# Optimization experiments

Measured on AMD Instinct MI355X. Metric: run time of the kernel, lower is better.

The kernel has to match this reference:

```python
import jax, jax.numpy as jnp
import numpy as np

C_IN = 256
C_INT = C_IN // 2  # inter_channels


def _conv1x1(x, w, b):
    # x: [B, Cin, H, W], w: [Cout, Cin], b: [Cout]
    return jnp.einsum('bchw,oc->bohw', x, w) + b[None, :, None, None]


def setup_inputs() -> dict:
    key = jax.random.key(0)
    ks = jax.random.split(key, 9)
    B, H, W = 8, 64, 64
    s_in = 1.0 / np.sqrt(C_IN)
    s_int = 1.0 / np.sqrt(C_INT)
    return {
        'x': jax.random.normal(ks[0], (B, C_IN, H, W), dtype=jnp.float32),
        'g_w': jax.random.normal(ks[1], (C_INT, C_IN), dtype=jnp.float32) * s_in,
        'g_b': jax.random.normal(ks[2], (C_INT,), dtype=jnp.float32) * s_in,
        'theta_w': jax.random.normal(ks[3], (C_INT, C_IN), dtype=jnp.float32) * s_in,
        'theta_b': jax.random.normal(ks[4], (C_INT,), dtype=jnp.float32) * s_in,
        'phi_w': jax.random.normal(ks[5], (C_INT, C_IN), dtype=jnp.float32) * s_in,
        'phi_b': jax.random.normal(ks[6], (C_INT,), dtype=jnp.float32) * s_in,
        'W_w': jax.random.normal(ks[7], (C_IN, C_INT), dtype=jnp.float32) * s_int,
        'W_b': jax.random.normal(ks[8], (C_IN,), dtype=jnp.float32) * s_int,
    }


def reference(x, g_w, g_b, theta_w, theta_b, phi_w, phi_b, W_w, W_b):
    B, C, H, W = x.shape
    N = H * W
    g_x = _conv1x1(x, g_w, g_b).reshape(B, C_INT, N)        # [B, Ci, N]
    theta_x = _conv1x1(x, theta_w, theta_b).reshape(B, C_INT, N)
    phi_x = _conv1x1(x, phi_w, phi_b).reshape(B, C_INT, N)
    # f[b, i, j] = theta[:, i] . phi[:, j]  (no scaling, per original)
    f = jnp.einsum('bci,bcj->bij', theta_x, phi_x)          # [B, N, N]
    f_div_C = jax.nn.softmax(f, axis=-1)
    y = jnp.einsum('bij,bcj->bci', f_div_C, g_x)            # [B, Ci, N]
    y = y.reshape(B, C_INT, H, W)
    y = _conv1x1(y, W_w, W_b)                               # [B, C, H, W]
    return x + y
```

## Files before the change

kernel.cpp:

```cpp
#include <hip/hip_runtime.h>

typedef _Float16 f16;
typedef _Float16 f16x2 __attribute__((ext_vector_type(2)));
typedef _Float16 f16x4 __attribute__((ext_vector_type(4)));
typedef _Float16 f16x8 __attribute__((ext_vector_type(8)));
typedef float f32x4 __attribute__((ext_vector_type(4)));
typedef float f32x16 __attribute__((ext_vector_type(16)));

#define MFMA16(a, b, c) __builtin_amdgcn_mfma_f32_16x16x32_f16(a, b, c, 0, 0, 0)
#define MFMA32(a, b, c) __builtin_amdgcn_mfma_f32_32x32x16_f16(a, b, c, 0, 0, 0)

__device__ __forceinline__ int swzr(int row) { return ((row & 7) << 4) ^ ((row & 8) << 2); }

__global__ __launch_bounds__(256) void wcvt_k(
    const float* __restrict__ tw, const float* __restrict__ pw,
    const float* __restrict__ gw, const float* __restrict__ ww,
    f16* __restrict__ Wall, f16* __restrict__ Wepi) {
  int i = blockIdx.x * 256 + threadIdx.x;
  if (i < 384 * 256) {
    int c = i >> 8, cp = i & 255;
    float v = (c < 128) ? tw[c * 256 + cp]
            : (c < 256) ? pw[(c - 128) * 256 + cp]
                        : gw[(c - 256) * 256 + cp];
    Wall[i] = (f16)v;
  }
  int j = i - 384 * 256;
  if (j >= 0 && j < 256 * 128) Wepi[j] = (f16)ww[j];
}

__global__ __launch_bounds__(256) void xpose_k(const float* __restrict__ x,
                                               f16* __restrict__ xT) {
  __shared__ f16 t[64 * 65];
  int bx = blockIdx.x;
  int b = bx >> 8, rem = bx & 255;
  int c0 = (rem >> 6) * 64, n0 = (rem & 63) * 64;
  const float* xb = x + ((size_t)b * 256 + c0) * 4096 + n0;
#pragma unroll
  for (int rep = 0; rep < 16; ++rep) {
    int idx = rep * 256 + threadIdx.x;
    int i = idx >> 6, j = idx & 63;
    t[j * 65 + i] = (f16)xb[(size_t)i * 4096 + j];
  }
  __syncthreads();
  f16* o = xT + ((size_t)b * 4096 + n0) * 256 + c0;
#pragma unroll
  for (int rep = 0; rep < 16; ++rep) {
    int idx = rep * 256 + threadIdx.x;
    int j = idx >> 6, i = idx & 63;
    o[(size_t)j * 256 + i] = t[j * 65 + i];
  }
}

__global__ __launch_bounds__(256) void proj_k(
    const f16* __restrict__ xT, const f16* __restrict__ Wall,
    const float* __restrict__ tb, const float* __restrict__ pb,
    const float* __restrict__ gb, f16* __restrict__ Q, f16* __restrict__ K,
    f16* __restrict__ Vt) {
  __shared__ f16 vs[128 * 65];
  int b = blockIdx.x >> 6, nt = blockIdx.x & 63;
  int nbase = nt * 64;
  int w = threadIdx.x >> 6, lane = threadIdx.x & 63;
  int lr = lane & 15, lhi = lane >> 4;
  int nrow = nbase + w * 16 + lr;
  const f16x8* xr = (const f16x8*)(xT + ((size_t)b * 4096 + nrow) * 256);
  f16x8 a[8];
#pragma unroll
  for (int ks = 0; ks < 8; ++ks) a[ks] = xr[ks * 4 + lhi];
  f32x4 acc[24];
#pragma unroll
  for (int ct = 0; ct < 24; ++ct) {
    acc[ct] = {0.f, 0.f, 0.f, 0.f};
    const f16x8* wr = (const f16x8*)(Wall + (size_t)(ct * 16 + lr) * 256);
#pragma unroll
    for (int ks = 0; ks < 8; ++ks) acc[ct] = MFMA16(a[ks], wr[ks * 4 + lhi], acc[ct]);
  }
  int nloc = w * 16 + lhi * 4;
#pragma unroll
  for (int ct = 0; ct < 24; ++ct) {
    int c = ct * 16 + lr;
    float bias = (c < 128) ? tb[c] : (c < 256) ? pb[c - 128] : gb[c - 256];
#pragma unroll
    for (int r = 0; r < 4; ++r) {
      float v = acc[ct][r] + bias;
      int n = nbase + nloc + r;
      if (c < 128)
        Q[((size_t)b * 4096 + n) * 128 + c] = (f16)v;
      else if (c < 256)
        K[((size_t)b * 4096 + n) * 128 + (c - 128)] = (f16)v;
      else
        vs[(c - 256) * 65 + nloc + r] = (f16)v;
    }
  }
  __syncthreads();
  f16* vo = Vt + (size_t)b * 128 * 4096 + nbase;
  for (int rep = 0; rep < 32; ++rep) {
    int idx = rep * 256 + threadIdx.x;
    int c = idx >> 6, j = idx & 63;
    vo[(size_t)c * 4096 + j] = vs[c * 65 + j];
  }
}

__global__ __launch_bounds__(256, 2) void attn_k(const f16* __restrict__ Q,
                                                 const f16* __restrict__ K,
                                                 const f16* __restrict__ Vt,
                                                 f16* __restrict__ Yp,
                                                 float2* __restrict__ ml) {
  __shared__ f16 Ks[2][64 * 128];
  __shared__ f16 Vs[2][128 * 64];
  const float L = 1.44269504f;
  int swzid = ((blockIdx.x & 7) << 6) | ((int)blockIdx.x >> 3);
  int b = swzid >> 6, rem = swzid & 63;
  int qt = rem >> 1, half = rem & 1;
  int qbase = qt * 128;
  int kvbase = half * 2048;
  int tid = threadIdx.x;
  int w = tid >> 6, lane = tid & 63;
  int col = lane & 31, hi = lane >> 5;

  const f16* Qr = Q + ((size_t)b * 4096 + qbase + w * 32 + col) * 128;
  f16x8 bq[8];
#pragma unroll
  for (int ks = 0; ks < 8; ++ks) bq[ks] = *(const f16x8*)(Qr + ks * 16 + hi * 8);

  f32x16 yacc[4];
#pragma unroll
  for (int dt = 0; dt < 4; ++dt)
#pragma unroll
    for (int r = 0; r < 16; ++r) yacc[dt][r] = 0.f;
  float m = -1e30f, l = 0.f, nmL = 1e30f;

  const f16* Kbase = K + (size_t)b * 4096 * 128;
  const f16* Vbase = Vt + (size_t)b * 128 * 4096;

  int krow = tid >> 4, kcolb = (tid & 15) * 16;
  int vrow = tid >> 1, h2 = tid & 1;
  int sv = swzr(vrow);

  int vblo[4];
#pragma unroll
  for (int u = 0; u < 4; ++u) vblo[u] = h2 * 64 + (u & 2) * 16 + (u & 1) * 8;

  {
    const f16* Kt = Kbase + (size_t)kvbase * 128;
    f16x8 kr[4], vr[4];
#pragma unroll
    for (int r = 0; r < 4; ++r) kr[r] = *(const f16x8*)(Kt + (r * 256 + tid) * 8);
#pragma unroll
    for (int u = 0; u < 4; ++u)
      vr[u] = *(const f16x8*)(Vbase + (size_t)vrow * 4096 + kvbase + h2 * 32 + u * 8);
#pragma unroll
    for (int r = 0; r < 4; ++r) {
      int row = r * 16 + krow;
      *(f16x8*)((char*)Ks[0] + row * 256 + (kcolb ^ swzr(row))) = kr[r];
    }
#pragma unroll
    for (int u = 0; u < 4; ++u) {
      f16x4 lo = {vr[u][0], vr[u][1], vr[u][2], vr[u][3]};
      f16x4 hi4 = {vr[u][4], vr[u][5], vr[u][6], vr[u][7]};
      *(f16x4*)((char*)Vs[0] + vrow * 128 + (vblo[u] ^ sv)) = lo;
      *(f16x4*)((char*)Vs[0] + vrow * 128 + ((vblo[u] + 16) ^ sv)) = hi4;
    }
  }

  for (int t = 0; t < 32; ++t) {
    int cur = t & 1, nxt = cur ^ 1;
    f16x8 kr[4], vr[4];
    bool pf = (t + 1 < 32);
    if (pf) {
      int kv0 = kvbase + (t + 1) * 64;
      const f16* Kt = Kbase + (size_t)kv0 * 128;
#pragma unroll
      for (int r = 0; r < 4; ++r) kr[r] = *(const f16x8*)(Kt + (r * 256 + tid) * 8);
#pragma unroll
      for (int u = 0; u < 4; ++u)
        vr[u] = *(const f16x8*)(Vbase + (size_t)vrow * 4096 + kv0 + h2 * 32 + u * 8);
    }
    __syncthreads();

    f32x16 s2[2];
    __builtin_amdgcn_s_setprio(1);
#pragma unroll
    for (int t2 = 0; t2 < 2; ++t2) {
#pragma unroll
      for (int r = 0; r < 16; ++r) s2[t2][r] = 0.f;
      int row = t2 * 32 + col;
      const char* kb = (const char*)Ks[cur] + row * 256;
      int sk = swzr(row);
#pragma unroll
      for (int ks = 0; ks < 8; ++ks) {
        f16x8 ak = *(const f16x8*)(kb + ((ks * 32 + hi * 16) ^ sk));
        s2[t2] = MFMA32(ak, bq[ks], s2[t2]);
      }
    }
    __builtin_amdgcn_s_setprio(0);

    float v[16];
#pragma unroll
    for (int r = 0; r < 16; ++r) v[r] = fmaxf(s2[0][r], s2[1][r]);
#pragma unroll
    for (int st = 8; st > 0; st >>= 1)
#pragma unroll
      for (int i = 0; i < 16; ++i)
        if (i < st) v[i] = fmaxf(v[i], v[i + st]);
    float pm = v[0];
    pm = fmaxf(pm, __shfl_xor(pm, 32));
    if (pm > m + 8.f) {
      float sc = __expf(m - pm);
      m = pm;
      nmL = -m * L;
      l *= sc;
#pragma unroll
      for (int dt = 0; dt < 4; ++dt)
#pragma unroll
        for (int r = 0; r < 16; ++r) yacc[dt][r] *= sc;
    }
#pragma unroll
    for (int t2 = 0; t2 < 2; ++t2)
#pragma unroll
      for (int r = 0; r < 16; ++r) s2[t2][r] = exp2f(fmaf(s2[t2][r], L, nmL));
    float sv16[16];
#pragma unroll
    for (int r = 0; r < 16; ++r) sv16[r] = s2[0][r] + s2[1][r];
#pragma unroll
    for (int st = 8; st > 0; st >>= 1)
#pragma unroll
      for (int i = 0; i < 16; ++i)
        if (i < st) sv16[i] += sv16[i + st];
    float rs = sv16[0];
    rs += __shfl_xor(rs, 32);
    l += rs;

    f16x8 pfr[4];
#pragma unroll
    for (int t2 = 0; t2 < 2; ++t2)
#pragma unroll
      for (int k1 = 0; k1 < 2; ++k1) {
        f16x8 f;
#pragma unroll
        for (int c = 0; c < 8; ++c) f[c] = (f16)s2[t2][8 * k1 + c];
        pfr[t2 * 2 + k1] = f;
      }

    __builtin_amdgcn_s_setprio(1);
#pragma unroll
    for (int kstep = 0; kstep < 4; ++kstep) {
#pragma unroll
      for (int dt = 0; dt < 4; ++dt) {
        int row = dt * 32 + col;
        f16x8 av = *(const f16x8*)((const char*)Vs[cur] + row * 128 +
                                   ((kstep * 32 + hi * 16) ^ swzr(row)));
        yacc[dt] = MFMA32(av, pfr[kstep], yacc[dt]);
      }
    }
    __builtin_amdgcn_s_setprio(0);

    if (pf) {
#pragma unroll
      for (int r = 0; r < 4; ++r) {
        int row = r * 16 + krow;
        *(f16x8*)((char*)Ks[nxt] + row * 256 + (kcolb ^ swzr(row))) = kr[r];
      }
#pragma unroll
      for (int u = 0; u < 4; ++u) {
        f16x4 lo = {vr[u][0], vr[u][1], vr[u][2], vr[u][3]};
        f16x4 hi4 = {vr[u][4], vr[u][5], vr[u][6], vr[u][7]};
        *(f16x4*)((char*)Vs[nxt] + vrow * 128 + (vblo[u] ^ sv)) = lo;
        *(f16x4*)((char*)Vs[nxt] + vrow * 128 + ((vblo[u] + 16) ^ sv)) = hi4;
      }
    }
  }

  size_t rowYp = (size_t)half * 32768 + (size_t)b * 4096 + qbase + w * 32 + col;
  float inv = 1.0f / l;
  f16* yo = Yp + rowYp * 128;
#pragma unroll
  for (int dt = 0; dt < 4; ++dt)
#pragma unroll
    for (int a = 0; a < 4; ++a) {
      f16x4 ov = {(f16)(yacc[dt][4 * a] * inv), (f16)(yacc[dt][4 * a + 1] * inv),
                  (f16)(yacc[dt][4 * a + 2] * inv), (f16)(yacc[dt][4 * a + 3] * inv)};
      *(f16x4*)(yo + dt * 32 + a * 8 + hi * 4) = ov;
    }
  if (hi == 0) ml[rowYp] = make_float2(m, l);
}

__global__ __launch_bounds__(256) void comb_k(const f16* __restrict__ Yp,
                                              const float2* __restrict__ ml,
                                              f16* __restrict__ Y) {
  int row = blockIdx.x * 16 + (threadIdx.x >> 4);
  int e = (threadIdx.x & 15) * 8;
  float2 ml0 = ml[row], ml1 = ml[32768 + row];
  float m = fmaxf(ml0.x, ml1.x);
  float w0 = ml0.y * __expf(ml0.x - m), w1 = ml1.y * __expf(ml1.x - m);
  float inv = 1.f / (w0 + w1);
  w0 *= inv;
  w1 *= inv;
  f16x8 a = *(const f16x8*)(Yp + (size_t)row * 128 + e);
  f16x8 c = *(const f16x8*)(Yp + (size_t)(32768 + row) * 128 + e);
  f16x8 o;
#pragma unroll
  for (int i = 0; i < 8; ++i) o[i] = (f16)(w0 * (float)a[i] + w1 * (float)c[i]);
  *(f16x8*)(Y + (size_t)row * 128 + e) = o;
}

__global__ __launch_bounds__(256) void epi_k(const f16* __restrict__ Y,
                                             const f16* __restrict__ Wepi,
                                             const float* __restrict__ Wb,
                                             const float* __restrict__ x,
                                             float* __restrict__ out) {
  int b = blockIdx.x >> 6, nt = blockIdx.x & 63;
  int nbase = nt * 64;
  int w = threadIdx.x >> 6, lane = threadIdx.x & 63;
  int lr = lane & 15, lhi = lane >> 4;
  f16x8 by[4][4];
#pragma unroll
  for (int n4 = 0; n4 < 4; ++n4) {
    const f16x8* yr = (const f16x8*)(Y + ((size_t)b * 4096 + nbase + n4 * 16 + lr) * 128);
#pragma unroll
    for (int ks = 0; ks < 4; ++ks) by[n4][ks] = yr[ks * 4 + lhi];
  }
#pragma unroll
  for (int ot = 0; ot < 4; ++ot) {
    int o0 = w * 64 + ot * 16;
    const f16x8* wr = (const f16x8*)(Wepi + (size_t)(o0 + lr) * 128);
    f16x8 a[4];
#pragma unroll
    for (int ks = 0; ks < 4; ++ks) a[ks] = wr[ks * 4 + lhi];
#pragma unroll
    for (int n4 = 0; n4 < 4; ++n4) {
      f32x4 acc = {0.f, 0.f, 0.f, 0.f};
#pragma unroll
      for (int ks = 0; ks < 4; ++ks) acc = MFMA16(a[ks], by[n4][ks], acc);
#pragma unroll
      for (int r = 0; r < 4; ++r) {
        int o = o0 + lhi * 4 + r;
        int n = nbase + n4 * 16 + lr;
        size_t idx = ((size_t)b * 256 + o) * 4096 + n;
        out[idx] = x[idx] + Wb[o] + acc[r];
      }
    }
  }
}

extern "C" void kernel_launch(void* const* d_in, const int* in_sizes, int n_in,
                              void* d_out, int out_size, void* d_ws, size_t ws_size,
                              hipStream_t stream) {
  const float* x       = (const float*)d_in[0];
  const float* g_w     = (const float*)d_in[1];
  const float* g_b     = (const float*)d_in[2];
  const float* theta_w = (const float*)d_in[3];
  const float* theta_b = (const float*)d_in[4];
  const float* phi_w   = (const float*)d_in[5];
  const float* phi_b   = (const float*)d_in[6];
  const float* W_w     = (const float*)d_in[7];
  const float* W_b     = (const float*)d_in[8];
  float* out = (float*)d_out;

  f16* xT   = (f16*)d_ws;
  f16* Q    = xT + (size_t)8 * 4096 * 256;
  f16* Kk   = Q + (size_t)8 * 4096 * 128;
  f16* Vt   = Kk + (size_t)8 * 4096 * 128;
  f16* Wall = Vt + (size_t)8 * 4096 * 128;
  f16* Wepi = Wall + 384 * 256;
  float2* ml = (float2*)(Wepi + 256 * 128);
  f16* Yp   = xT;
  f16* Y    = Q;

  wcvt_k<<<512, 256, 0, stream>>>(theta_w, phi_w, g_w, W_w, Wall, Wepi);
  xpose_k<<<2048, 256, 0, stream>>>(x, xT);
  proj_k<<<512, 256, 0, stream>>>(xT, Wall, theta_b, phi_b, g_b, Q, Kk, Vt);
  attn_k<<<512, 256, 0, stream>>>(Q, Kk, Vt, Yp, ml);
  comb_k<<<2048, 256, 0, stream>>>(Yp, ml, Y);
  epi_k<<<512, 256, 0, stream>>>(Y, Wepi, W_b, x, out);
}
```

Before: 195.2 us.

## Split attention KV into four chunks, fuse combine into epilogue, single-buffer LDS

The attention kernel now splits each query tile's KV range four ways instead of two, launching twice as many blocks with a single LDS buffer and an occupancy hint of 4 blocks per CU. The separate combine kernel is removed: the epilogue merges the four partial outputs using the stored max and sum values before its MFMA projection. The per-iteration row-sum reduction is deferred to the end, and the max reduction is flattened. The aim is more parallelism and occupancy and one fewer launch, at the cost of an extra barrier per iteration and more partial-output memory traffic. That traffic uses a new buffer placed in the workspace after ml.

Result: slower. 656.4 us (+236.2%).

```diff
diff --git a/kernel.cpp b/kernel.cpp
--- a/kernel.cpp
+++ b/kernel.cpp
@@ -100,19 +100,20 @@
   }
 }
 
-__global__ __launch_bounds__(256, 2) void attn_k(const f16* __restrict__ Q,
+__global__ __launch_bounds__(256, 4) void attn_k(const f16* __restrict__ Q,
                                                  const f16* __restrict__ K,
                                                  const f16* __restrict__ Vt,
-                                                 f16* __restrict__ Yp,
+                                                 f16* __restrict__ Yp01,
+                                                 f16* __restrict__ Yp23,
                                                  float2* __restrict__ ml) {
-  __shared__ f16 Ks[2][64 * 128];
-  __shared__ f16 Vs[2][128 * 64];
+  __shared__ f16 Ks[64 * 128];
+  __shared__ f16 Vs[128 * 64];
   const float L = 1.44269504f;
-  int swzid = ((blockIdx.x & 7) << 6) | ((int)blockIdx.x >> 3);
-  int b = swzid >> 6, rem = swzid & 63;
-  int qt = rem >> 1, half = rem & 1;
+  int swzid = ((blockIdx.x & 7) << 7) | ((int)blockIdx.x >> 3);
+  int b = swzid >> 7, rem = swzid & 127;
+  int qt = rem >> 2, s = rem & 3;
   int qbase = qt * 128;
-  int kvbase = half * 2048;
+  int kvbase = s << 10;
   int tid = threadIdx.x;
   int w = tid >> 6, lane = tid & 63;
   int col = lane & 31, hi = lane >> 5;
@@ -127,7 +128,10 @@
   for (int dt = 0; dt < 4; ++dt)
 #pragma unroll
     for (int r = 0; r < 16; ++r) yacc[dt][r] = 0.f;
-  float m = -1e30f, l = 0.f, nmL = 1e30f;
+  float lv[16];
+#pragma unroll
+  for (int r = 0; r < 16; ++r) lv[r] = 0.f;
+  float m = -1e30f, nmL = 1e30f;
 
   const f16* Kbase = K + (size_t)b * 4096 * 128;
   const f16* Vbase = Vt + (size_t)b * 128 * 4096;
@@ -135,7 +139,6 @@
   int krow = tid >> 4, kcolb = (tid & 15) * 16;
   int vrow = tid >> 1, h2 = tid & 1;
   int sv = swzr(vrow);
-
   int vblo[4];
 #pragma unroll
   for (int u = 0; u < 4; ++u) vblo[u] = h2 * 64 + (u & 2) * 16 + (u & 1) * 8;
@@ -151,21 +154,20 @@
 #pragma unroll
     for (int r = 0; r < 4; ++r) {
       int row = r * 16 + krow;
-      *(f16x8*)((char*)Ks[0] + row * 256 + (kcolb ^ swzr(row))) = kr[r];
+      *(f16x8*)((char*)Ks + row * 256 + (kcolb ^ swzr(row))) = kr[r];
     }
 #pragma unroll
     for (int u = 0; u < 4; ++u) {
       f16x4 lo = {vr[u][0], vr[u][1], vr[u][2], vr[u][3]};
       f16x4 hi4 = {vr[u][4], vr[u][5], vr[u][6], vr[u][7]};
-      *(f16x4*)((char*)Vs[0] + vrow * 128 + (vblo[u] ^ sv)) = lo;
-      *(f16x4*)((char*)Vs[0] + vrow * 128 + ((vblo[u] + 16) ^ sv)) = hi4;
-    }
-  }
-
-  for (int t = 0; t < 32; ++t) {
-    int cur = t & 1, nxt = cur ^ 1;
+      *(f16x4*)((char*)Vs + vrow * 128 + (vblo[u] ^ sv)) = lo;
+      *(f16x4*)((char*)Vs + vrow * 128 + ((vblo[u] + 16) ^ sv)) = hi4;
+    }
+  }
+
+  for (int t = 0; t < 16; ++t) {
     f16x8 kr[4], vr[4];
-    bool pf = (t + 1 < 32);
+    bool pf = (t + 1 < 16);
     if (pf) {
       int kv0 = kvbase + (t + 1) * 64;
       const f16* Kt = Kbase + (size_t)kv0 * 128;
@@ -184,7 +186,7 @@
 #pragma unroll
       for (int r = 0; r < 16; ++r) s2[t2][r] = 0.f;
       int row = t2 * 32 + col;
-      const char* kb = (const char*)Ks[cur] + row * 256;
+      const char* kb = (const char*)Ks + row * 256;
       int sk = swzr(row);
 #pragma unroll
       for (int ks = 0; ks < 8; ++ks) {
@@ -197,48 +199,42 @@
     float v[16];
 #pragma unroll
     for (int r = 0; r < 16; ++r) v[r] = fmaxf(s2[0][r], s2[1][r]);
-#pragma unroll
-    for (int st = 8; st > 0; st >>= 1)
-#pragma unroll
-      for (int i = 0; i < 16; ++i)
-        if (i < st) v[i] = fmaxf(v[i], v[i + st]);
-    float pm = v[0];
+    float t0 = fmaxf(fmaxf(v[0], v[1]), v[2]);
+    float t1 = fmaxf(fmaxf(v[3], v[4]), v[5]);
+    float t2 = fmaxf(fmaxf(v[6], v[7]), v[8]);
+    float t3 = fmaxf(fmaxf(v[9], v[10]), v[11]);
+    float t4 = fmaxf(fmaxf(v[12], v[13]), v[14]);
+    float u0 = fmaxf(fmaxf(t0, t1), t2);
+    float u1 = fmaxf(fmaxf(t3, t4), v[15]);
+    float pm = fmaxf(u0, u1);
     pm = fmaxf(pm, __shfl_xor(pm, 32));
     if (pm > m + 8.f) {
       float sc = __expf(m - pm);
       m = pm;
       nmL = -m * L;
-      l *= sc;
+#pragma unroll
+      for (int r = 0; r < 16; ++r) lv[r] *= sc;
 #pragma unroll
       for (int dt = 0; dt < 4; ++dt)
 #pragma unroll
         for (int r = 0; r < 16; ++r) yacc[dt][r] *= sc;
     }
 #pragma unroll
-    for (int t2 = 0; t2 < 2; ++t2)
-#pragma unroll
-      for (int r = 0; r < 16; ++r) s2[t2][r] = exp2f(fmaf(s2[t2][r], L, nmL));
-    float sv16[16];
-#pragma unroll
-    for (int r = 0; r < 16; ++r) sv16[r] = s2[0][r] + s2[1][r];
-#pragma unroll
-    for (int st = 8; st > 0; st >>= 1)
-#pragma unroll
-      for (int i = 0; i < 16; ++i)
-        if (i < st) sv16[i] += sv16[i + st];
-    float rs = sv16[0];
-    rs += __shfl_xor(rs, 32);
-    l += rs;
+    for (int t2i = 0; t2i < 2; ++t2i)
+#pragma unroll
+      for (int r = 0; r < 16; ++r) s2[t2i][r] = exp2f(fmaf(s2[t2i][r], L, nmL));
+#pragma unroll
+    for (int r = 0; r < 16; ++r) lv[r] += s2[0][r] + s2[1][r];
 
     f16x8 pfr[4];
 #pragma unroll
-    for (int t2 = 0; t2 < 2; ++t2)
+    for (int t2i = 0; t2i < 2; ++t2i)
 #pragma unroll
       for (int k1 = 0; k1 < 2; ++k1) {
         f16x8 f;
 #pragma unroll
-        for (int c = 0; c < 8; ++c) f[c] = (f16)s2[t2][8 * k1 + c];
-        pfr[t2 * 2 + k1] = f;
+        for (int c = 0; c < 8; ++c) f[c] = (f16)s2[t2i][8 * k1 + c];
+        pfr[t2i * 2 + k1] = f;
       }
 
     __builtin_amdgcn_s_setprio(1);
@@ -247,32 +243,41 @@
 #pragma unroll
       for (int dt = 0; dt < 4; ++dt) {
         int row = dt * 32 + col;
-        f16x8 av = *(const f16x8*)((const char*)Vs[cur] + row * 128 +
+        f16x8 av = *(const f16x8*)((const char*)Vs + row * 128 +
                                    ((kstep * 32 + hi * 16) ^ swzr(row)));
         yacc[dt] = MFMA32(av, pfr[kstep], yacc[dt]);
       }
     }
     __builtin_amdgcn_s_setprio(0);
 
+    __syncthreads();
     if (pf) {
 #pragma unroll
       for (int r = 0; r < 4; ++r) {
         int row = r * 16 + krow;
-        *(f16x8*)((char*)Ks[nxt] + row * 256 + (kcolb ^ swzr(row))) = kr[r];
+        *(f16x8*)((char*)Ks + row * 256 + (kcolb ^ swzr(row))) = kr[r];
       }
 #pragma unroll
       for (int u = 0; u < 4; ++u) {
         f16x4 lo = {vr[u][0], vr[u][1], vr[u][2], vr[u][3]};
         f16x4 hi4 = {vr[u][4], vr[u][5], vr[u][6], vr[u][7]};
-        *(f16x4*)((char*)Vs[nxt] + vrow * 128 + (vblo[u] ^ sv)) = lo;
-        *(f16x4*)((char*)Vs[nxt] + vrow * 128 + ((vblo[u] + 16) ^ sv)) = hi4;
-      }
-    }
-  }
-
-  size_t rowYp = (size_t)half * 32768 + (size_t)b * 4096 + qbase + w * 32 + col;
+        *(f16x4*)((char*)Vs + vrow * 128 + (vblo[u] ^ sv)) = lo;
+        *(f16x4*)((char*)Vs + vrow * 128 + ((vblo[u] + 16) ^ sv)) = hi4;
+      }
+    }
+  }
+
+  float l8[8], l4[4];
+#pragma unroll
+  for (int i = 0; i < 8; ++i) l8[i] = lv[i] + lv[i + 8];
+#pragma unroll
+  for (int i = 0; i < 4; ++i) l4[i] = l8[i] + l8[i + 4];
+  float l = (l4[0] + l4[1]) + (l4[2] + l4[3]);
+  l += __shfl_xor(l, 32);
+
+  int rowG = b * 4096 + qbase + w * 32 + col;
+  f16* yo = (s < 2 ? Yp01 : Yp23) + ((size_t)(s & 1) * 32768 + rowG) * 128;
   float inv = 1.0f / l;
-  f16* yo = Yp + rowYp * 128;
 #pragma unroll
   for (int dt = 0; dt < 4; ++dt)
 #pragma unroll
@@ -281,29 +286,12 @@
                   (f16)(yacc[dt][4 * a + 2] * inv), (f16)(yacc[dt][4 * a + 3] * inv)};
       *(f16x4*)(yo + dt * 32 + a * 8 + hi * 4) = ov;
     }
-  if (hi == 0) ml[rowYp] = make_float2(m, l);
-}
-
-__global__ __launch_bounds__(256) void comb_k(const f16* __restrict__ Yp,
-                                              const float2* __restrict__ ml,
-                                              f16* __restrict__ Y) {
-  int row = blockIdx.x * 16 + (threadIdx.x >> 4);
-  int e = (threadIdx.x & 15) * 8;
-  float2 ml0 = ml[row], ml1 = ml[32768 + row];
-  float m = fmaxf(ml0.x, ml1.x);
-  float w0 = ml0.y * __expf(ml0.x - m), w1 = ml1.y * __expf(ml1.x - m);
-  float inv = 1.f / (w0 + w1);
-  w0 *= inv;
-  w1 *= inv;
-  f16x8 a = *(const f16x8*)(Yp + (size_t)row * 128 + e);
-  f16x8 c = *(const f16x8*)(Yp + (size_t)(32768 + row) * 128 + e);
-  f16x8 o;
-#pragma unroll
-  for (int i = 0; i < 8; ++i) o[i] = (f16)(w0 * (float)a[i] + w1 * (float)c[i]);
-  *(f16x8*)(Y + (size_t)row * 128 + e) = o;
-}
-
-__global__ __launch_bounds__(256) void epi_k(const f16* __restrict__ Y,
+  if (hi == 0) ml[s * 32768 + rowG] = make_float2(m, l);
+}
+
+__global__ __launch_bounds__(256) void epi_k(const f16* __restrict__ Yp01,
+                                             const f16* __restrict__ Yp23,
+                                             const float2* __restrict__ ml,
                                              const f16* __restrict__ Wepi,
                                              const float* __restrict__ Wb,
                                              const float* __restrict__ x,
@@ -312,12 +300,35 @@
   int nbase = nt * 64;
   int w = threadIdx.x >> 6, lane = threadIdx.x & 63;
   int lr = lane & 15, lhi = lane >> 4;
+  const f16* yb0 = Yp01;
+  const f16* yb1 = Yp01 + (size_t)32768 * 128;
+  const f16* yb2 = Yp23;
+  const f16* yb3 = Yp23 + (size_t)32768 * 128;
   f16x8 by[4][4];
 #pragma unroll
   for (int n4 = 0; n4 < 4; ++n4) {
-    const f16x8* yr = (const f16x8*)(Y + ((size_t)b * 4096 + nbase + n4 * 16 + lr) * 128);
-#pragma unroll
-    for (int ks = 0; ks < 4; ++ks) by[n4][ks] = yr[ks * 4 + lhi];
+    int row = b * 4096 + nbase + n4 * 16 + lr;
+    float2 m0 = ml[row], m1 = ml[32768 + row], m2 = ml[65536 + row], m3 = ml[98304 + row];
+    float mm = fmaxf(fmaxf(m0.x, m1.x), fmaxf(m2.x, m3.x));
+    float w0 = m0.y * __expf(m0.x - mm), w1 = m1.y * __expf(m1.x - mm);
+    float w2 = m2.y * __expf(m2.x - mm), w3 = m3.y * __expf(m3.x - mm);
+    float inv = 1.f / (w0 + w1 + w2 + w3);
+    w0 *= inv; w1 *= inv; w2 *= inv; w3 *= inv;
+    size_t rb = (size_t)row * 128;
+#pragma unroll
+    for (int ks = 0; ks < 4; ++ks) {
+      int eo = ks * 32 + lhi * 8;
+      f16x8 a0 = *(const f16x8*)(yb0 + rb + eo);
+      f16x8 a1 = *(const f16x8*)(yb1 + rb + eo);
+      f16x8 a2 = *(const f16x8*)(yb2 + rb + eo);
+      f16x8 a3 = *(const f16x8*)(yb3 + rb + eo);
+      f16x8 o;
+#pragma unroll
+      for (int e = 0; e < 8; ++e)
+        o[e] = (f16)(w0 * (float)a0[e] + w1 * (float)a1[e] + w2 * (float)a2[e] +
+                     w3 * (float)a3[e]);
+      by[n4][ks] = o;
+    }
   }
 #pragma unroll
   for (int ot = 0; ot < 4; ++ot) {
@@ -363,13 +374,12 @@
   f16* Wall = Vt + (size_t)8 * 4096 * 128;
   f16* Wepi = Wall + 384 * 256;
   float2* ml = (float2*)(Wepi + 256 * 128);
-  f16* Yp   = xT;
-  f16* Y    = Q;
+  f16* Yp23 = (f16*)(ml + 4 * 32768);
+  f16* Yp01 = xT;
 
   wcvt_k<<<512, 256, 0, stream>>>(theta_w, phi_w, g_w, W_w, Wall, Wepi);
   xpose_k<<<2048, 256, 0, stream>>>(x, xT);
   proj_k<<<512, 256, 0, stream>>>(xT, Wall, theta_b, phi_b, g_b, Q, Kk, Vt);
-  attn_k<<<512, 256, 0, stream>>>(Q, Kk, Vt, Yp, ml);
-  comb_k<<<2048, 256, 0, stream>>>(Yp, ml, Y);
-  epi_k<<<512, 256, 0, stream>>>(Y, Wepi, W_b, x, out);
-}
+  attn_k<<<1024, 256, 0, stream>>>(Q, Kk, Vt, Yp01, Yp23, ml);
+  epi_k<<<512, 256, 0, stream>>>(Yp01, Yp23, ml, Wepi, W_b, x, out);
+}
```
